# Kernel optimization log

Hardware: AMD Instinct MI355X
Metric: run time of the kernel (lower is better)

## Reference

```python
import jax, jax.numpy as jnp
import numpy as np

# Faithful notes on the original torch code:
# - MLP path with n_networks=1: angles = MLP(coeffs), shape [N,1]. Dropout is
#   eval-mode identity (dropout=0.0).
# - aggregate_k_hop: step_k is a single buffer that torch_scatter ACCUMULATES into
#   across hops (scatter(..., out=step_k) adds into out), and enhanced_angles
#   ALIASES angles, so `enhanced_angles += step_k` mutates the angle vector that
#   is read at the next hop. We reproduce both behaviors.
# - k-hop paths are deduplicated via np.unique, i.e. the scatter at hop k sums
#   angles[dest] over UNIQUE (src,dest) pairs reachable in exactly k edge steps.
#   That is exactly the boolean k-th power of the adjacency matrix, so we use
#   dense boolean matrix powers (static shapes, jit-friendly) instead of the
#   dynamic-shape unique() roundtrip.

N_NODES = 4096
IN_DIM = 128
N_EDGES = 131072
K_HOPS = 3


def setup_inputs() -> dict:
    key = jax.random.key(0)
    ks = jax.random.split(key, 8)
    coeffs = jax.random.normal(ks[0], (N_NODES, IN_DIM), dtype=jnp.float32)
    edge_index = jax.random.randint(ks[1], (2, N_EDGES), 0, N_NODES, dtype=jnp.int64)
    # Xavier-normal linear weights (torch layout: [out, in])
    def xavier(k, out_d, in_d):
        std = np.sqrt(2.0 / (in_d + out_d)).astype(np.float32)
        return jax.random.normal(k, (out_d, in_d), dtype=jnp.float32) * std
    W0 = xavier(ks[2], IN_DIM, IN_DIM)
    b0 = jnp.zeros((IN_DIM,), jnp.float32)
    W1 = xavier(ks[3], IN_DIM, IN_DIM)  # use_bias=False
    W2 = xavier(ks[4], IN_DIM, IN_DIM)
    W3 = xavier(ks[5], 1, IN_DIM)
    b3 = jnp.zeros((1,), jnp.float32)
    return {"coeffs": coeffs, "edge_index": edge_index,
            "W0": W0, "b0": b0, "W1": W1, "W2": W2, "W3": W3, "b3": b3}


def reference(coeffs, edge_index, W0, b0, W1, W2, W3, b3):
    n = coeffs.shape[0]
    h = jax.nn.relu(coeffs @ W0.T + b0)
    h = jax.nn.relu(h @ W1.T)
    h = jax.nn.relu(h @ W2.T)
    a = h @ W3.T + b3  # [N, 1]

    # ---- aggregate_k_hop (k=3), f(k) = log(k+1) ----
    row, col = edge_index[0], edge_index[1]
    # hop 1: raw edge list scatter (duplicates kept, as in the original)
    step = jax.ops.segment_sum(a[col] * jnp.float32(np.log(2.0)), row,
                               num_segments=n)  # [N,1]
    a = a + step
    # hops >= 2: unique k-step paths == boolean adjacency power
    A = jnp.zeros((n, n), jnp.bool_).at[row, col].set(True)
    Af = A.astype(jnp.float32)
    Ak = Af
    for k_ in range(2, K_HOPS + 1):
        Ak = ((Ak @ Af) > 0).astype(jnp.float32)  # unique k_-hop reachability
        step = step + jnp.float32(np.log(k_ + 1.0)) * (Ak @ a)
        a = a + step
    return a
```

## Files before the change

kernel.cpp:

```cpp
#include <hip/hip_runtime.h>
#include <cstdint>
#include <cstddef>


constexpr int NN   = 4096;
constexpr int D    = 128;
constexpr int NE   = 131072;
constexpr int WPR  = 64;
constexpr int MAXN = 256;

typedef __attribute__((ext_vector_type(8))) short  short8;
typedef __attribute__((ext_vector_type(4))) float  float4v;

__device__ __forceinline__ unsigned short f32_bf16(float x) {
  unsigned u = __float_as_uint(x);
  return (unsigned short)((u + 0x7FFFu + ((u >> 16) & 1u)) >> 16);
}
__device__ __forceinline__ float bf16_f32(unsigned short b) {
  return __uint_as_float(((unsigned)b) << 16);
}

struct Frag { short8 hi; short8 lo; };

__device__ __forceinline__ Frag split8(const float* __restrict__ p) {
  float4v a = *(const float4v*)p;
  float4v b = *(const float4v*)(p + 4);
  Frag f;
#pragma unroll
  for (int j = 0; j < 4; ++j) {
    float x = a[j];
    unsigned short h = f32_bf16(x);
    f.hi[j] = (short)h;
    f.lo[j] = (short)f32_bf16(x - bf16_f32(h));
    float y = b[j];
    unsigned short h2 = f32_bf16(y);
    f.hi[j + 4] = (short)h2;
    f.lo[j + 4] = (short)f32_bf16(y - bf16_f32(h2));
  }
  return f;
}

__device__ __forceinline__ float4v mfma3(const Frag& A, const Frag& B, float4v c) {
  c = __builtin_amdgcn_mfma_f32_16x16x32_bf16(A.lo, B.hi, c, 0, 0, 0);
  c = __builtin_amdgcn_mfma_f32_16x16x32_bf16(A.hi, B.lo, c, 0, 0, 0);
  c = __builtin_amdgcn_mfma_f32_16x16x32_bf16(A.hi, B.hi, c, 0, 0, 0);
  return c;
}

__device__ __forceinline__ float wave_sum64(float v) {
#pragma unroll
  for (int off = 32; off >= 1; off >>= 1) v += __shfl_xor(v, off, 64);
  return v;
}

__global__ __launch_bounds__(256) void pack_w(
    const float* __restrict__ W0, const float* __restrict__ W1,
    const float* __restrict__ W2, short* __restrict__ Wp) {
  int tid = blockIdx.x * 256 + threadIdx.x;
  int lane = tid & 63, kt = (tid >> 6) & 3, o = (tid >> 8) & 7, L = tid >> 11;
  int quad = lane >> 4, l16 = lane & 15;
  const float* W = (L == 0) ? W0 : (L == 1) ? W1 : W2;
  Frag f = split8(W + (size_t)(o * 16 + l16) * D + kt * 32 + quad * 8);
  short* base = Wp + (size_t)(((L * 8 + o) * 4) + kt) * 1024;
  *(short8*)(base + lane * 8) = f.hi;
  *(short8*)(base + 512 + lane * 8) = f.lo;
}

__global__ __launch_bounds__(256) void mlp_mfma(
    const float* __restrict__ coeffs, const short* __restrict__ Wp,
    const float* __restrict__ b0,
    const float* __restrict__ W3, const float* __restrict__ b3,
    float* __restrict__ a0v,
    unsigned long long* __restrict__ A, float* __restrict__ s1,
    float* __restrict__ ws2) {
  __shared__ float hbuf[16 * 132];
  __shared__ float psh[4][16];
  const int b = blockIdx.x, t = threadIdx.x;
  const int wave = t >> 6, lane = t & 63;
  const int quad = lane >> 4, l16 = lane & 15;
  const int node0 = b * 8;
  const int ot0 = 2 * wave, ot1 = 2 * wave + 1;

  {
    float4v z4 = {0.f, 0.f, 0.f, 0.f};
    ((float4v*)A)[(size_t)b * 256 + t] = z4;
    if (t < 2) ((float4v*)(s1 + node0))[t] = z4;
    if (b == 0 && t < 16) ((float4v*)ws2)[t] = z4;
  }

  float4v r0, r1;
#pragma unroll
  for (int L = 0; L < 3; ++L) {
    Frag Af[4];
    const float* abase = (L == 0)
        ? coeffs + (size_t)(node0 + (l16 & 7)) * D + quad * 8
        : hbuf + (l16 & 7) * 132 + quad * 8;
#pragma unroll
    for (int kt = 0; kt < 4; ++kt) Af[kt] = split8(abase + kt * 32);
    const short* WL = Wp + (size_t)L * 8 * 4 * 1024;
    float4v acc0 = {0.f, 0.f, 0.f, 0.f}, acc1 = acc0;
#pragma unroll
    for (int kt = 0; kt < 4; ++kt) {
      const short* p0 = WL + (size_t)(ot0 * 4 + kt) * 1024 + lane * 8;
      const short* p1 = WL + (size_t)(ot1 * 4 + kt) * 1024 + lane * 8;
      Frag B0, B1;
      B0.hi = *(const short8*)p0;
      B0.lo = *(const short8*)(p0 + 512);
      B1.hi = *(const short8*)p1;
      B1.lo = *(const short8*)(p1 + 512);
      acc0 = mfma3(Af[kt], B0, acc0);
      acc1 = mfma3(Af[kt], B1, acc1);
    }
    if (L == 0) {
      float ba = b0[ot0 * 16 + l16], bb = b0[ot1 * 16 + l16];
#pragma unroll
      for (int j = 0; j < 4; ++j) { acc0[j] += ba; acc1[j] += bb; }
    }
#pragma unroll
    for (int j = 0; j < 4; ++j) {
      acc0[j] = fmaxf(acc0[j], 0.f);
      acc1[j] = fmaxf(acc1[j], 0.f);
    }
    if (L < 2) {
      __syncthreads();
#pragma unroll
      for (int j = 0; j < 4; ++j) {
        hbuf[(quad * 4 + j) * 132 + ot0 * 16 + l16] = acc0[j];
        hbuf[(quad * 4 + j) * 132 + ot1 * 16 + l16] = acc1[j];
      }
      __syncthreads();
    } else {
      r0 = acc0; r1 = acc1;
    }
  }
  float w3a = W3[ot0 * 16 + l16], w3b = W3[ot1 * 16 + l16];
#pragma unroll
  for (int j = 0; j < 4; ++j) {
    float v = fmaf(r0[j], w3a, r1[j] * w3b);
#pragma unroll
    for (int off = 1; off <= 8; off <<= 1) v += __shfl_xor(v, off, 64);
    if (l16 == 0) psh[wave][quad * 4 + j] = v;
  }
  __syncthreads();
  if (t < 8)
    a0v[node0 + t] = psh[0][t] + psh[1][t] + psh[2][t] + psh[3][t] + b3[0];
}

__global__ __launch_bounds__(256) void build_graph(
    const int* __restrict__ er, const int* __restrict__ ec,
    const float* __restrict__ a0, unsigned long long* __restrict__ A,
    float* __restrict__ s1) {
  int e = blockIdx.x * 256 + threadIdx.x;
  if (e >= NE) return;
  int r = er[e] & (NN - 1);
  int c = ec[e] & (NN - 1);
  atomicOr(&A[(size_t)r * WPR + (c >> 6)], 1ull << (c & 63));
  atomicAdd(&s1[r], a0[c] * 0.6931471805599453f);
}

__global__ __launch_bounds__(256) void a1_ws(
    const float* __restrict__ a0, const float* __restrict__ s1,
    float* __restrict__ a1, float* __restrict__ ws1) {
  int t = threadIdx.x, i = blockIdx.x * 256 + t;
  float v = a0[i] + s1[i];
  a1[i] = v;
  float s = wave_sum64(v);
  if ((t & 63) == 0) ws1[i >> 6] = s;
}

__device__ __forceinline__ void stage_v(const float* __restrict__ v,
                                        float* __restrict__ vl, int t) {
#pragma unroll
  for (int u = 0; u < 16; ++u) {
    int j = t + u * 256;
    vl[(j >> 6) * 65 + (j & 63)] = v[j];
  }
}

__device__ __forceinline__ unsigned long long gather_row(
    const unsigned long long* __restrict__ Arow,
    const unsigned long long* __restrict__ SRC,
    int i, int lane, unsigned short* __restrict__ nbr, int* __restrict__ ncnt) {
  if (lane == 0) *ncnt = 0;
  unsigned long long rw = Arow[(size_t)i * WPR + lane];
  int c = __popcll(rw);
  int base = 0;
  if (c) base = atomicAdd(ncnt, c);
  while (rw) {
    int b = __builtin_ctzll(rw);
    rw &= rw - 1ull;
    if (base < MAXN) nbr[base] = (unsigned short)((lane << 6) + b);
    ++base;
  }
  int cnt = *ncnt;
  cnt = cnt < MAXN ? cnt : MAXN;
  unsigned long long acc = 0ull;
  int j = 0;
  for (; j + 8 <= cnt; j += 8) {
    unsigned long long v0 = SRC[(size_t)nbr[j + 0] * WPR + lane];
    unsigned long long v1 = SRC[(size_t)nbr[j + 1] * WPR + lane];
    unsigned long long v2 = SRC[(size_t)nbr[j + 2] * WPR + lane];
    unsigned long long v3 = SRC[(size_t)nbr[j + 3] * WPR + lane];
    unsigned long long v4 = SRC[(size_t)nbr[j + 4] * WPR + lane];
    unsigned long long v5 = SRC[(size_t)nbr[j + 5] * WPR + lane];
    unsigned long long v6 = SRC[(size_t)nbr[j + 6] * WPR + lane];
    unsigned long long v7 = SRC[(size_t)nbr[j + 7] * WPR + lane];
    acc |= ((v0 | v1) | (v2 | v3)) | ((v4 | v5) | (v6 | v7));
  }
  for (; j < cnt; ++j) acc |= SRC[(size_t)nbr[j] * WPR + lane];
  return acc;
}

__device__ __forceinline__ float masked_dot(
    unsigned long long m, const float* __restrict__ vl,
    const float* __restrict__ wsum, int lane) {
  int cnt = __popcll(m);
  bool inv = cnt > 32;
  unsigned long long it = inv ? ~m : m;
  float part = inv ? wsum[lane] : 0.f;
  float sgn = inv ? -1.f : 1.f;
  const float* p = vl + lane * 65;
  float acc = 0.f;
  while (it) {
    int b = __builtin_ctzll(it);
    it &= it - 1ull;
    acc += p[b];
  }
  return fmaf(sgn, acc, part);
}

__global__ __launch_bounds__(256) void hop2(
    const unsigned long long* __restrict__ A, unsigned long long* __restrict__ A2,
    const float* __restrict__ a1, const float* __restrict__ ws1,
    const float* __restrict__ s1, float* __restrict__ s2, float* __restrict__ a2,
    float* __restrict__ ws2) {
  __shared__ float vl[64 * 65];
  __shared__ unsigned short nbr[4][MAXN];
  __shared__ int ncnt[4];
  int t = threadIdx.x, wave = t >> 6, lane = t & 63;
  stage_v(a1, vl, t);
  __syncthreads();
  int i = blockIdx.x * 4 + wave;
  unsigned long long acc = gather_row(A, A, i, lane, nbr[wave], &ncnt[wave]);
  A2[(size_t)i * WPR + lane] = acc;
  float part = masked_dot(acc, vl, ws1, lane);
  part = wave_sum64(part);
  if (lane == 0) {
    float s2v = fmaf(1.0986122886681098f, part, s1[i]);
    s2[i] = s2v;
    float a2v = a1[i] + s2v;
    a2[i] = a2v;
    atomicAdd(&ws2[i >> 6], a2v);
  }
}

__global__ __launch_bounds__(256) void hop3(
    const unsigned long long* __restrict__ A, const unsigned long long* __restrict__ A2,
    const float* __restrict__ a2, const float* __restrict__ ws2,
    const float* __restrict__ s2, float* __restrict__ out) {
  __shared__ float vl[64 * 65];
  __shared__ unsigned short nbr[4][MAXN];
  __shared__ int ncnt[4];
  int t = threadIdx.x, wave = t >> 6, lane = t & 63;
  stage_v(a2, vl, t);
  __syncthreads();
  int i = blockIdx.x * 4 + wave;
  unsigned long long acc = gather_row(A, A2, i, lane, nbr[wave], &ncnt[wave]);
  float part = masked_dot(acc, vl, ws2, lane);
  part = wave_sum64(part);
  if (lane == 0)
    out[i] = a2[i] + fmaf(1.3862943611198906f, part, s2[i]);
}

extern "C" void kernel_launch(void* const* d_in, const int* in_sizes, int n_in,
                              void* d_out, int out_size, void* d_ws, size_t ws_size,
                              hipStream_t stream) {
  const float* coeffs = (const float*)d_in[0];
  const int*   edge   = (const int*)d_in[1];
  const float* W0 = (const float*)d_in[2];
  const float* b0 = (const float*)d_in[3];
  const float* W1 = (const float*)d_in[4];
  const float* W2 = (const float*)d_in[5];
  const float* W3 = (const float*)d_in[6];
  const float* b3 = (const float*)d_in[7];
  float* out = (float*)d_out;

  char* ws = (char*)d_ws;
  unsigned long long* A  = (unsigned long long*)ws;
  unsigned long long* A2 = (unsigned long long*)(ws + (2u << 20));
  float* f   = (float*)(ws + (4u << 20));
  float* a0v = f;
  float* a1v = f + 4096;
  float* s1  = f + 8192;
  float* s2  = f + 12288;
  float* a2v = f + 16384;
  float* ws1 = f + 20480;
  float* ws2 = f + 20544;
  short* Wp  = (short*)(ws + (4u << 20) + 128 * 1024);

  pack_w<<<24, 256, 0, stream>>>(W0, W1, W2, Wp);
  mlp_mfma<<<NN / 8, 256, 0, stream>>>(coeffs, Wp, b0, W3, b3, a0v, A, s1, ws2);
  build_graph<<<NE / 256, 256, 0, stream>>>(edge, edge + NE, a0v, A, s1);
  a1_ws<<<NN / 256, 256, 0, stream>>>(a0v, s1, a1v, ws1);
  hop2<<<NN / 4, 256, 0, stream>>>(A, A2, a1v, ws1, s1, s2, a2v, ws2);
  hop3<<<NN / 4, 256, 0, stream>>>(A, A2, a2v, ws2, s2, out);
}
```

Measured before the change: 141.6 us.

## Fuse a1 computation and word sums into hop kernels, drop a1_ws launch

Removes the separate a1_ws kernel: hop2 now builds a1 = a0 + s1 while staging into shared memory, and both hop kernels compute the per-64-node word sums locally instead of reading a global ws1/ws2 built by atomics. This eliminates one launch and the global atomicAdd into ws2, at the cost of every block redundantly recomputing 4096 sums. The MLP kernel also hoists weight fragment loads ahead of the activation loads and adds a min-blocks occupancy hint.

Result: faster. 117.5 us (median of 2 runs) (-17.0%).

```diff
diff --git a/kernel.cpp b/kernel.cpp
--- a/kernel.cpp
+++ b/kernel.cpp
@@ -22,9 +22,7 @@
 
 struct Frag { short8 hi; short8 lo; };
 
-__device__ __forceinline__ Frag split8(const float* __restrict__ p) {
-  float4v a = *(const float4v*)p;
-  float4v b = *(const float4v*)(p + 4);
+__device__ __forceinline__ Frag mk_frag(float4v a, float4v b) {
   Frag f;
 #pragma unroll
   for (int j = 0; j < 4; ++j) {
@@ -38,6 +36,9 @@
     f.lo[j + 4] = (short)f32_bf16(y - bf16_f32(h2));
   }
   return f;
+}
+__device__ __forceinline__ Frag split8(const float* __restrict__ p) {
+  return mk_frag(*(const float4v*)p, *(const float4v*)(p + 4));
 }
 
 __device__ __forceinline__ float4v mfma3(const Frag& A, const Frag& B, float4v c) {
@@ -66,13 +67,12 @@
   *(short8*)(base + 512 + lane * 8) = f.lo;
 }
 
-__global__ __launch_bounds__(256) void mlp_mfma(
+__global__ __launch_bounds__(256, 2) void mlp_mfma(
     const float* __restrict__ coeffs, const short* __restrict__ Wp,
     const float* __restrict__ b0,
     const float* __restrict__ W3, const float* __restrict__ b3,
     float* __restrict__ a0v,
-    unsigned long long* __restrict__ A, float* __restrict__ s1,
-    float* __restrict__ ws2) {
+    unsigned long long* __restrict__ A, float* __restrict__ s1) {
   __shared__ float hbuf[16 * 132];
   __shared__ float psh[4][16];
   const int b = blockIdx.x, t = threadIdx.x;
@@ -85,29 +85,43 @@
     float4v z4 = {0.f, 0.f, 0.f, 0.f};
     ((float4v*)A)[(size_t)b * 256 + t] = z4;
     if (t < 2) ((float4v*)(s1 + node0))[t] = z4;
-    if (b == 0 && t < 16) ((float4v*)ws2)[t] = z4;
   }
 
   float4v r0, r1;
 #pragma unroll
   for (int L = 0; L < 3; ++L) {
-    Frag Af[4];
-    const float* abase = (L == 0)
-        ? coeffs + (size_t)(node0 + (l16 & 7)) * D + quad * 8
-        : hbuf + (l16 & 7) * 132 + quad * 8;
-#pragma unroll
-    for (int kt = 0; kt < 4; ++kt) Af[kt] = split8(abase + kt * 32);
-    const short* WL = Wp + (size_t)L * 8 * 4 * 1024;
-    float4v acc0 = {0.f, 0.f, 0.f, 0.f}, acc1 = acc0;
+    const short* WL = Wp + (size_t)L * 32768;
+    short8 Bf[4][4];
 #pragma unroll
     for (int kt = 0; kt < 4; ++kt) {
       const short* p0 = WL + (size_t)(ot0 * 4 + kt) * 1024 + lane * 8;
       const short* p1 = WL + (size_t)(ot1 * 4 + kt) * 1024 + lane * 8;
-      Frag B0, B1;
-      B0.hi = *(const short8*)p0;
-      B0.lo = *(const short8*)(p0 + 512);
-      B1.hi = *(const short8*)p1;
-      B1.lo = *(const short8*)(p1 + 512);
+      Bf[kt][0] = *(const short8*)p0;
+      Bf[kt][1] = *(const short8*)(p0 + 512);
+      Bf[kt][2] = *(const short8*)p1;
+      Bf[kt][3] = *(const short8*)(p1 + 512);
+    }
+    Frag Af[4];
+    if (L == 0) {
+      const float* abase = coeffs + (size_t)(node0 + (l16 & 7)) * D + quad * 8;
+      float4v araw[8];
+#pragma unroll
+      for (int kt = 0; kt < 4; ++kt) {
+        araw[2 * kt]     = *(const float4v*)(abase + kt * 32);
+        araw[2 * kt + 1] = *(const float4v*)(abase + kt * 32 + 4);
+      }
+#pragma unroll
+      for (int kt = 0; kt < 4; ++kt) Af[kt] = mk_frag(araw[2 * kt], araw[2 * kt + 1]);
+    } else {
+      const float* abase = hbuf + (l16 & 7) * 132 + quad * 8;
+#pragma unroll
+      for (int kt = 0; kt < 4; ++kt) Af[kt] = split8(abase + kt * 32);
+    }
+    float4v acc0 = {0.f, 0.f, 0.f, 0.f}, acc1 = acc0;
+#pragma unroll
+    for (int kt = 0; kt < 4; ++kt) {
+      Frag B0; B0.hi = Bf[kt][0]; B0.lo = Bf[kt][1];
+      Frag B1; B1.hi = Bf[kt][2]; B1.lo = Bf[kt][3];
       acc0 = mfma3(Af[kt], B0, acc0);
       acc1 = mfma3(Af[kt], B1, acc1);
     }
@@ -156,25 +170,6 @@
   int c = ec[e] & (NN - 1);
   atomicOr(&A[(size_t)r * WPR + (c >> 6)], 1ull << (c & 63));
   atomicAdd(&s1[r], a0[c] * 0.6931471805599453f);
-}
-
-__global__ __launch_bounds__(256) void a1_ws(
-    const float* __restrict__ a0, const float* __restrict__ s1,
-    float* __restrict__ a1, float* __restrict__ ws1) {
-  int t = threadIdx.x, i = blockIdx.x * 256 + t;
-  float v = a0[i] + s1[i];
-  a1[i] = v;
-  float s = wave_sum64(v);
-  if ((t & 63) == 0) ws1[i >> 6] = s;
-}
-
-__device__ __forceinline__ void stage_v(const float* __restrict__ v,
-                                        float* __restrict__ vl, int t) {
-#pragma unroll
-  for (int u = 0; u < 16; ++u) {
-    int j = t + u * 256;
-    vl[(j >> 6) * 65 + (j & 63)] = v[j];
-  }
 }
 
 __device__ __forceinline__ unsigned long long gather_row(
@@ -229,47 +224,70 @@
   return fmaf(sgn, acc, part);
 }
 
+__device__ __forceinline__ void word_sums(const float* __restrict__ vl,
+                                          float* __restrict__ wsm, int t) {
+  if (t < 64) {
+    float s = 0.f;
+    const float* p = vl + t * 65;
+#pragma unroll 16
+    for (int b2 = 0; b2 < 64; ++b2) s += p[b2];
+    wsm[t] = s;
+  }
+}
+
 __global__ __launch_bounds__(256) void hop2(
     const unsigned long long* __restrict__ A, unsigned long long* __restrict__ A2,
-    const float* __restrict__ a1, const float* __restrict__ ws1,
-    const float* __restrict__ s1, float* __restrict__ s2, float* __restrict__ a2,
-    float* __restrict__ ws2) {
+    const float* __restrict__ a0, const float* __restrict__ s1,
+    float* __restrict__ s2, float* __restrict__ a2) {
   __shared__ float vl[64 * 65];
+  __shared__ float wsm[64];
   __shared__ unsigned short nbr[4][MAXN];
   __shared__ int ncnt[4];
   int t = threadIdx.x, wave = t >> 6, lane = t & 63;
-  stage_v(a1, vl, t);
+#pragma unroll
+  for (int u = 0; u < 16; ++u) {
+    int j = t + u * 256;
+    vl[(j >> 6) * 65 + (j & 63)] = a0[j] + s1[j];
+  }
+  __syncthreads();
+  word_sums(vl, wsm, t);
   __syncthreads();
   int i = blockIdx.x * 4 + wave;
   unsigned long long acc = gather_row(A, A, i, lane, nbr[wave], &ncnt[wave]);
   A2[(size_t)i * WPR + lane] = acc;
-  float part = masked_dot(acc, vl, ws1, lane);
+  float part = masked_dot(acc, vl, wsm, lane);
   part = wave_sum64(part);
   if (lane == 0) {
     float s2v = fmaf(1.0986122886681098f, part, s1[i]);
     s2[i] = s2v;
-    float a2v = a1[i] + s2v;
-    a2[i] = a2v;
-    atomicAdd(&ws2[i >> 6], a2v);
+    a2[i] = vl[(i >> 6) * 65 + (i & 63)] + s2v;
   }
 }
 
 __global__ __launch_bounds__(256) void hop3(
     const unsigned long long* __restrict__ A, const unsigned long long* __restrict__ A2,
-    const float* __restrict__ a2, const float* __restrict__ ws2,
-    const float* __restrict__ s2, float* __restrict__ out) {
+    const float* __restrict__ a2, const float* __restrict__ s2,
+    float* __restrict__ out) {
   __shared__ float vl[64 * 65];
+  __shared__ float wsm[64];
   __shared__ unsigned short nbr[4][MAXN];
   __shared__ int ncnt[4];
   int t = threadIdx.x, wave = t >> 6, lane = t & 63;
-  stage_v(a2, vl, t);
+#pragma unroll
+  for (int u = 0; u < 16; ++u) {
+    int j = t + u * 256;
+    vl[(j >> 6) * 65 + (j & 63)] = a2[j];
+  }
+  __syncthreads();
+  word_sums(vl, wsm, t);
   __syncthreads();
   int i = blockIdx.x * 4 + wave;
   unsigned long long acc = gather_row(A, A2, i, lane, nbr[wave], &ncnt[wave]);
-  float part = masked_dot(acc, vl, ws2, lane);
+  float part = masked_dot(acc, vl, wsm, lane);
   part = wave_sum64(part);
   if (lane == 0)
-    out[i] = a2[i] + fmaf(1.3862943611198906f, part, s2[i]);
+    out[i] = vl[(i >> 6) * 65 + (i & 63)] +
+             fmaf(1.3862943611198906f, part, s2[i]);
 }
 
 extern "C" void kernel_launch(void* const* d_in, const int* in_sizes, int n_in,
@@ -290,18 +308,14 @@
   unsigned long long* A2 = (unsigned long long*)(ws + (2u << 20));
   float* f   = (float*)(ws + (4u << 20));
   float* a0v = f;
-  float* a1v = f + 4096;
-  float* s1  = f + 8192;
-  float* s2  = f + 12288;
-  float* a2v = f + 16384;
-  float* ws1 = f + 20480;
-  float* ws2 = f + 20544;
+  float* s1  = f + 4096;
+  float* s2  = f + 8192;
+  float* a2v = f + 12288;
   short* Wp  = (short*)(ws + (4u << 20) + 128 * 1024);
 
   pack_w<<<24, 256, 0, stream>>>(W0, W1, W2, Wp);
-  mlp_mfma<<<NN / 8, 256, 0, stream>>>(coeffs, Wp, b0, W3, b3, a0v, A, s1, ws2);
+  mlp_mfma<<<NN / 8, 256, 0, stream>>>(coeffs, Wp, b0, W3, b3, a0v, A, s1);
   build_graph<<<NE / 256, 256, 0, stream>>>(edge, edge + NE, a0v, A, s1);
-  a1_ws<<<NN / 256, 256, 0, stream>>>(a0v, s1, a1v, ws1);
-  hop2<<<NN / 4, 256, 0, stream>>>(A, A2, a1v, ws1, s1, s2, a2v, ws2);
-  hop3<<<NN / 4, 256, 0, stream>>>(A, A2, a2v, ws2, s2, out);
-}
+  hop2<<<NN / 4, 256, 0, stream>>>(A, A2, a0v, s1, s2, a2v);
+  hop3<<<NN / 4, 256, 0, stream>>>(A, A2, a2v, s2, out);
+}
```
